# Performance work log

Hardware: AMD Instinct MI355X
Metric: run time of the kernel (lower is better)

## Reference

```python
import jax, jax.numpy as jnp
import numpy as np

NEG = -9e15  # mask value used by dense GAT implementations
BN_EPS = 1e-5


def gat_layer(x, W, a_src, a_dst, adj_mask):
    # Dense-adjacency GAT layer (pyGAT GraphAttentionLayer math).
    Wh = x @ W                                              # [N, H]
    e = jax.nn.leaky_relu(
        (Wh @ a_src)[:, None] + (Wh @ a_dst)[None, :], 0.2)  # [N, N]
    scores = jnp.where(adj_mask, e, NEG)
    att = jax.nn.softmax(scores, axis=1)                    # scatter-softmax over neighbors
    return att @ Wh                                         # [N, H]


def batchnorm(h, gamma, beta):
    # BatchNorm1d in training mode: biased batch stats over the node axis.
    mu = h.mean(axis=0)
    var = h.var(axis=0)
    return gamma * (h - mu) * jax.lax.rsqrt(var + BN_EPS) + beta


def setup_inputs() -> dict:
    key = jax.random.key(0)
    ks = jax.random.split(key, 8)
    N, F, H = 4096, 512, 256
    x = jax.random.normal(ks[0], (N, F), dtype=jnp.float32)
    adj = jax.random.randint(ks[1], (N, N), 0, 2, dtype=jnp.int32)
    W1 = jax.random.normal(ks[2], (F, H), dtype=jnp.float32) / np.sqrt(F)
    a1_src = jax.random.normal(ks[3], (H,), dtype=jnp.float32) / np.sqrt(H)
    a1_dst = jax.random.normal(ks[4], (H,), dtype=jnp.float32) / np.sqrt(H)
    W2 = jax.random.normal(ks[5], (H, H), dtype=jnp.float32) / np.sqrt(H)
    a2_src = jax.random.normal(ks[6], (H,), dtype=jnp.float32) / np.sqrt(H)
    a2_dst = jax.random.normal(ks[7], (H,), dtype=jnp.float32) / np.sqrt(H)
    return {
        "x": x, "adj": adj,
        "W1": W1, "a1_src": a1_src, "a1_dst": a1_dst,
        "gamma1": jnp.ones((H,), jnp.float32), "beta1": jnp.zeros((H,), jnp.float32),
        "W2": W2, "a2_src": a2_src, "a2_dst": a2_dst,
        "gamma2": jnp.ones((H,), jnp.float32), "beta2": jnp.zeros((H,), jnp.float32),
    }


def reference(x, adj, W1, a1_src, a1_dst, gamma1, beta1,
              W2, a2_src, a2_dst, gamma2, beta2):
    adj_mask = adj > 0
    h = jax.nn.relu(gat_layer(x, W1, a1_src, a1_dst, adj_mask))
    h = batchnorm(h, gamma1, beta1)
    # dropout is identity at inference time (deterministic reference)
    h = jax.nn.relu(gat_layer(h, W2, a2_src, a2_dst, adj_mask))
    h = batchnorm(h, gamma2, beta2)
    return h
```

## Files before the change

kernel.cpp:

```cpp
#include <hip/hip_runtime.h>

#define LOG2E 1.4426950408889634f

typedef unsigned long long u64;
typedef unsigned int uint;
typedef unsigned short ushort_t;
typedef __attribute__((ext_vector_type(8))) short short8;
typedef __attribute__((ext_vector_type(4))) float floatx4;
typedef __attribute__((ext_vector_type(4))) int intx4;
typedef __attribute__((ext_vector_type(4))) unsigned short ushort4v;

#define GN 4096
#define GH 256
#define KZ 8
#define KSTEPS 16

__device__ __forceinline__ ushort_t f2bf(float f){
  uint u = __float_as_uint(f);
  u += 0x7FFFu + ((u >> 16) & 1u);
  return (ushort_t)(u >> 16);
}
__device__ __forceinline__ float bf2f(ushort_t h){
  return __uint_as_float(((uint)h) << 16);
}
__device__ __forceinline__ float exp2_(float x){
#if __has_builtin(__builtin_amdgcn_exp2f)
  return __builtin_amdgcn_exp2f(x);
#else
  return exp2f(x);
#endif
}

__global__ __launch_bounds__(256) void prep(const int* __restrict__ adj,
                                            u64* __restrict__ mask,
                                            const float* __restrict__ W1,
                                            ushort_t* __restrict__ W1h,
                                            ushort_t* __restrict__ W1l,
                                            const float* __restrict__ W2,
                                            ushort_t* __restrict__ W2h,
                                            ushort_t* __restrict__ W2l){
  __shared__ union {
    unsigned char nib[2][1024];
    ushort_t tt[2][32][33];
  } sh;
  const int t = threadIdx.x;
  if (blockIdx.x < 2048){
    const int r0 = blockIdx.x * 2;
    const int* base = adj + (size_t)r0 * GN;
    #pragma unroll
    for (int i = 0; i < 8; ++i){
      int c = i * 256 + t;
      intx4 v = *(const intx4*)(base + c * 4);
      uint n = (uint)(v[0] > 0) | ((uint)(v[1] > 0) << 1) |
               ((uint)(v[2] > 0) << 2) | ((uint)(v[3] > 0) << 3);
      sh.nib[c >> 10][c & 1023] = (unsigned char)n;
    }
    __syncthreads();
    if (t < 128){
      int r = t >> 6, wi = t & 63;
      const u64* p = (const u64*)sh.nib[r];
      u64 x0 = p[wi * 2], x1 = p[wi * 2 + 1];
      auto comp = [](u64 x)->u64{
        x = (x | (x >> 4))  & 0x00FF00FF00FF00FFULL;
        x = (x | (x >> 8))  & 0x0000FFFF0000FFFFULL;
        x = (x | (x >> 16)) & 0x00000000FFFFFFFFULL;
        return x;
      };
      mask[(size_t)(r0 + r) * 64 + wi] = comp(x0) | (comp(x1) << 32);
    }
    return;
  }
  int b = blockIdx.x - 2048;
  const float* in; ushort_t* hi; ushort_t* lo; int R, idx;
  if (b < 128){ in = W1; hi = W1h; lo = W1l; R = 512; idx = b; }
  else        { in = W2; hi = W2h; lo = W2l; R = 256; idx = b - 128; }
  const int C = GH;
  const int bx = idx & 7, by = idx >> 3;
  const int i0 = by * 32, j0 = bx * 32;
  const int r = t >> 3, c4 = (t & 7) * 4;
  floatx4 v = *(const floatx4*)(in + (size_t)(i0 + r) * C + j0 + c4);
  #pragma unroll
  for (int e = 0; e < 4; ++e){
    ushort_t h = f2bf(v[e]);
    sh.tt[0][r][c4 + e] = h;
    sh.tt[1][r][c4 + e] = f2bf(v[e] - bf2f(h));
  }
  __syncthreads();
  ushort4v oh, ol;
  #pragma unroll
  for (int e = 0; e < 4; ++e){ oh[e] = sh.tt[0][c4 + e][r]; ol[e] = sh.tt[1][c4 + e][r]; }
  *(ushort4v*)(hi + (size_t)(j0 + r) * R + i0 + c4) = oh;
  *(ushort4v*)(lo + (size_t)(j0 + r) * R + i0 + c4) = ol;
}

template<bool BN>
__global__ __launch_bounds__(256) void gemm_split(const float* __restrict__ A,
                                                  const ushort_t* __restrict__ BThi,
                                                  const ushort_t* __restrict__ BTlo,
                                                  const float* __restrict__ bnsc,
                                                  const float* __restrict__ bnbi,
                                                  float* __restrict__ Cf, int K){
  __shared__ short8 AhiV[32 * 8];
  __shared__ short8 AloV[32 * 8];
  __shared__ short8 BhiV[64 * 8];
  __shared__ short8 BloV[64 * 8];
  char* Ahi = (char*)AhiV; char* Alo = (char*)AloV;
  char* Bhi = (char*)BhiV; char* Blo = (char*)BloV;
  const int tid = threadIdx.x;
  const int i0 = blockIdx.y * 32, n0 = blockIdx.x * 64;
  const int lane = tid & 63, wave = tid >> 6;
  const int wr = wave & 1, wc = wave >> 1;
  const int l15 = lane & 15, lhi = lane >> 4;
  const int rs = tid >> 3, ch = tid & 7;
  floatx4 acc[2] = {};
  for (int kb = 0; kb < K; kb += 64){
    {
      int r = rs;
      floatx4 f0 = *(const floatx4*)(A + (size_t)(i0 + r) * K + kb + ch * 8);
      floatx4 f1 = *(const floatx4*)(A + (size_t)(i0 + r) * K + kb + ch * 8 + 4);
      if constexpr (BN){
        floatx4 sc0 = *(const floatx4*)(bnsc + kb + ch * 8);
        floatx4 sc1 = *(const floatx4*)(bnsc + kb + ch * 8 + 4);
        floatx4 bi0 = *(const floatx4*)(bnbi + kb + ch * 8);
        floatx4 bi1 = *(const floatx4*)(bnbi + kb + ch * 8 + 4);
        #pragma unroll
        for (int e = 0; e < 4; ++e){
          f0[e] = f0[e] * sc0[e] + bi0[e];
          f1[e] = f1[e] * sc1[e] + bi1[e];
        }
      }
      short8 ah, al;
      #pragma unroll
      for (int e = 0; e < 4; ++e){
        ushort_t h0 = f2bf(f0[e]); ah[e] = (short)h0; al[e] = (short)f2bf(f0[e] - bf2f(h0));
        ushort_t h1 = f2bf(f1[e]); ah[e+4] = (short)h1; al[e+4] = (short)f2bf(f1[e] - bf2f(h1));
      }
      const int sw = (ch * 16) ^ ((r & 7) << 4);
      *(short8*)(Ahi + r * 128 + sw) = ah;
      *(short8*)(Alo + r * 128 + sw) = al;
      #pragma unroll
      for (int q = 0; q < 2; ++q){
        int rb = rs + q * 32;
        const int swb = (ch * 16) ^ ((rb & 7) << 4);
        short8 bh = *(const short8*)(BThi + (size_t)(n0 + rb) * K + kb + ch * 8);
        short8 bl = *(const short8*)(BTlo + (size_t)(n0 + rb) * K + kb + ch * 8);
        *(short8*)(Bhi + rb * 128 + swb) = bh;
        *(short8*)(Blo + rb * 128 + swb) = bl;
      }
    }
    __syncthreads();
    #pragma unroll
    for (int kt = 0; kt < 2; ++kt){
      int klb = (kt * 32 + lhi * 8) * 2;
      int rowA = wr * 16 + l15;
      int swA = klb ^ ((rowA & 7) << 4);
      short8 ah = *(const short8*)(Ahi + rowA * 128 + swA);
      short8 al = *(const short8*)(Alo + rowA * 128 + swA);
      #pragma unroll
      for (int n = 0; n < 2; ++n){
        int rowB = wc * 32 + n * 16 + l15;
        int swB = klb ^ ((rowB & 7) << 4);
        short8 bh = *(const short8*)(Bhi + rowB * 128 + swB);
        short8 bl = *(const short8*)(Blo + rowB * 128 + swB);
        acc[n] = __builtin_amdgcn_mfma_f32_16x16x32_bf16(ah, bh, acc[n], 0, 0, 0);
        acc[n] = __builtin_amdgcn_mfma_f32_16x16x32_bf16(ah, bl, acc[n], 0, 0, 0);
        acc[n] = __builtin_amdgcn_mfma_f32_16x16x32_bf16(al, bh, acc[n], 0, 0, 0);
      }
    }
    __syncthreads();
  }
  #pragma unroll
  for (int rr = 0; rr < 4; ++rr){
    int row = i0 + wr * 16 + lhi * 4 + rr;
    #pragma unroll
    for (int n = 0; n < 2; ++n){
      int col = n0 + wc * 32 + n * 16 + l15;
      Cf[(size_t)row * GH + col] = acc[n][rr];
    }
  }
}

__global__ __launch_bounds__(256) void skthi(const float* __restrict__ Whf,
                                             const float* __restrict__ asrc,
                                             const float* __restrict__ adst,
                                             float* __restrict__ ss,
                                             float* __restrict__ sd,
                                             ushort_t* __restrict__ VTh){
  __shared__ ushort_t tile[256][36];
  const int tid = threadIdx.x;
  const int i0 = blockIdx.x * 32;
  const int r = tid >> 3, cg = tid & 7;
  float s = 0.f, d = 0.f;
  #pragma unroll
  for (int j = 0; j < 8; ++j){
    int col = j * 32 + cg * 4;
    floatx4 v = *(const floatx4*)(Whf + (size_t)(i0 + r) * GH + col);
    floatx4 s4 = *(const floatx4*)(asrc + col);
    floatx4 d4 = *(const floatx4*)(adst + col);
    #pragma unroll
    for (int e = 0; e < 4; ++e){
      s += v[e] * s4[e]; d += v[e] * d4[e];
      tile[col + e][r] = f2bf(v[e]);
    }
  }
  #pragma unroll
  for (int off = 1; off < 8; off <<= 1){
    s += __shfl_xor(s, off);
    d += __shfl_xor(d, off);
  }
  if (cg == 0){ ss[i0 + r] = s * LOG2E; sd[i0 + r] = d * LOG2E; }
  __syncthreads();
  const int rr4 = (tid & 7) * 4, cb = tid >> 3;
  #pragma unroll
  for (int ct = 0; ct < 8; ++ct){
    int col = ct * 32 + cb;
    ushort4v o = *(const ushort4v*)(&tile[col][rr4]);
    *(ushort4v*)(VTh + (size_t)col * GN + i0 + rr4) = o;
  }
}

__global__ __launch_bounds__(128, 2) void gat_pv(const u64* __restrict__ mask,
                                                 const float* __restrict__ ss,
                                                 const float* __restrict__ sd,
                                                 const ushort_t* __restrict__ VTh,
                                                 float* __restrict__ partial,
                                                 float* __restrict__ szb){
  __shared__ char Blds[2][20480];
  const int tid = threadIdx.x;
  const int lane = tid & 63, w = tid >> 6;
  const int l15 = lane & 15, lhi = lane >> 4;
  const int i0 = blockIdx.x * 32;
  const int kz = blockIdx.y;
  const int ch = tid & 3, c0 = tid >> 2;
  const int ncol0 = w * 128;

  const int row0 = i0 + l15;
  const int row1 = i0 + 16 + l15;
  const float ss0 = ss[row0], ss1 = ss[row1];

  u64 mw0[8], mw1[8];
  {
    const u64* mr0 = mask + (size_t)row0 * 64 + kz * 8;
    const u64* mr1 = mask + (size_t)row1 * 64 + kz * 8;
    #pragma unroll
    for (int q = 0; q < 8; ++q){ mw0[q] = mr0[q]; mw1[q] = mr1[q]; }
  }

  floatx4 acc[2][8] = {};
  float srow0 = 0.f, srow1 = 0.f;
  short8 g[8];

  auto GLOAD = [&](int kb){
    const int kbase = (kz * KSTEPS + kb) * 32;
    #pragma unroll
    for (int i = 0; i < 8; ++i){
      int c = c0 + 32 * i;
      g[i] = *(const short8*)(VTh + (size_t)c * GN + kbase + ch * 8);
    }
  };
  auto SWRITE = [&](int buf){
    #pragma unroll
    for (int i = 0; i < 8; ++i){
      int c = c0 + 32 * i;
      *(short8*)(Blds[buf] + c * 80 + ch * 16) = g[i];
    }
  };

  GLOAD(0); SWRITE(0); __syncthreads();

  for (int kb = 0; kb < KSTEPS; ++kb){
    if (kb + 1 < KSTEPS) GLOAD(kb + 1);

    const int kbase = (kz * KSTEPS + kb) * 32;
    floatx4 s0 = *(const floatx4*)(sd + kbase + lhi * 8);
    floatx4 s1 = *(const floatx4*)(sd + kbase + lhi * 8 + 4);
    const int sh = ((kb & 1) << 5) + lhi * 8;
    uint b0 = (uint)(mw0[kb >> 1] >> sh) & 0xffu;
    uint b1 = (uint)(mw1[kb >> 1] >> sh) & 0xffu;
    short8 a0, a1;
    #pragma unroll
    for (int e = 0; e < 8; ++e){
      float sv = (e < 4) ? s0[e] : s1[e - 4];
      float t0 = ss0 + sv, t1 = ss1 + sv;
      float lr0 = fmaxf(t0, 0.2f * t0), lr1 = fmaxf(t1, 0.2f * t1);
      float p0 = exp2_(lr0), p1 = exp2_(lr1);
      p0 = ((b0 >> e) & 1u) ? p0 : 0.0f;
      p1 = ((b1 >> e) & 1u) ? p1 : 0.0f;
      srow0 += p0; srow1 += p1;
      a0[e] = (short)f2bf(p0);
      a1[e] = (short)f2bf(p1);
    }

    const char* B = Blds[kb & 1];
    #pragma unroll
    for (int n = 0; n < 8; ++n){
      short8 b = *(const short8*)(B + (ncol0 + n * 16 + l15) * 80 + lhi * 16);
      acc[0][n] = __builtin_amdgcn_mfma_f32_16x16x32_bf16(a0, b, acc[0][n], 0, 0, 0);
      acc[1][n] = __builtin_amdgcn_mfma_f32_16x16x32_bf16(a1, b, acc[1][n], 0, 0, 0);
    }

    if (kb + 1 < KSTEPS){
      SWRITE((kb + 1) & 1);
      __syncthreads();
    }
  }

  srow0 += __shfl_xor(srow0, 16); srow0 += __shfl_xor(srow0, 32);
  srow1 += __shfl_xor(srow1, 16); srow1 += __shfl_xor(srow1, 32);
  if (w == 0 && lhi == 0){
    szb[(size_t)kz * GN + row0] = srow0;
    szb[(size_t)kz * GN + row1] = srow1;
  }

  float* pout = partial + (size_t)kz * GN * GH;
  #pragma unroll
  for (int m = 0; m < 2; ++m){
    const int rbase = i0 + m * 16 + lhi * 4;
    #pragma unroll
    for (int n = 0; n < 8; ++n){
      int col = ncol0 + n * 16 + l15;
      #pragma unroll
      for (int rr = 0; rr < 4; ++rr)
        pout[(size_t)(rbase + rr) * GH + col] = acc[m][n][rr];
    }
  }
}

__global__ __launch_bounds__(256) void combine_colpart(const float* __restrict__ partial,
                                                       const float* __restrict__ szb,
                                                       float* __restrict__ outb,
                                                       float* __restrict__ part,
                                                       float* __restrict__ partm2){
  __shared__ float fl[4];
  __shared__ float sm[4][GH];
  const int tid = threadIdx.x;
  const int b = blockIdx.x;
  const int r0 = b * 4;
  if (tid < 4){
    int row = r0 + tid;
    float lsum = 0.f;
    #pragma unroll
    for (int z = 0; z < 8; ++z) lsum += szb[(size_t)z * GN + row];
    fl[tid] = lsum > 0.f ? 1.0f / lsum : 0.f;
  }
  __syncthreads();
  const int r = tid >> 6;
  const int c4 = (tid & 63) * 4;
  const size_t idx = (size_t)(r0 + r) * GH + c4;
  floatx4 x = {};
  #pragma unroll
  for (int z = 0; z < 8; ++z){
    floatx4 p = *(const floatx4*)(partial + (size_t)z * GN * GH + idx);
    #pragma unroll
    for (int e = 0; e < 4; ++e) x[e] += p[e];
  }
  const float linv = fl[r];
  #pragma unroll
  for (int e = 0; e < 4; ++e) x[e] = fmaxf(x[e] * linv, 0.0f);
  *(floatx4*)(outb + idx) = x;
  *(floatx4*)(&sm[r][c4]) = x;
  __syncthreads();
  if (tid < 64){
    const int cb = tid * 4;
    floatx4 v0 = *(const floatx4*)(&sm[0][cb]);
    floatx4 v1 = *(const floatx4*)(&sm[1][cb]);
    floatx4 v2 = *(const floatx4*)(&sm[2][cb]);
    floatx4 v3 = *(const floatx4*)(&sm[3][cb]);
    floatx4 s, m2;
    #pragma unroll
    for (int e = 0; e < 4; ++e){
      float sum = v0[e] + v1[e] + v2[e] + v3[e];
      float mu = sum * 0.25f;
      float d0 = v0[e]-mu, d1 = v1[e]-mu, d2 = v2[e]-mu, d3 = v3[e]-mu;
      s[e] = sum;
      m2[e] = d0*d0 + d1*d1 + d2*d2 + d3*d3;
    }
    *(floatx4*)(part + (size_t)b * GH + cb) = s;
    *(floatx4*)(partm2 + (size_t)b * GH + cb) = m2;
  }
}

__global__ __launch_bounds__(256) void colfin(const float* __restrict__ part,
                                              const float* __restrict__ partm2,
                                              const float* __restrict__ gamma,
                                              const float* __restrict__ beta,
                                              float* __restrict__ scale,
                                              float* __restrict__ bias){
  __shared__ double red[8][33];
  const int cl = threadIdx.x & 31, g = threadIdx.x >> 5;
  const int c = blockIdx.x * 32 + cl;
  double S = 0.0;
  for (int b = g * 128; b < g * 128 + 128; ++b) S += (double)part[(size_t)b * GH + c];
  red[g][cl] = S;
  __syncthreads();
  double mean = 0.0;
  #pragma unroll
  for (int q = 0; q < 8; ++q) mean += red[q][cl];
  mean *= (1.0 / 4096.0);
  double M2 = 0.0;
  for (int b = g * 128; b < g * 128 + 128; ++b){
    double mb = (double)part[(size_t)b * GH + c] * 0.25;
    double dd = mb - mean;
    M2 += (double)partm2[(size_t)b * GH + c] + 4.0 * dd * dd;
  }
  __syncthreads();
  red[g][cl] = M2;
  __syncthreads();
  if (g == 0){
    double M2t = 0.0;
    #pragma unroll
    for (int q = 0; q < 8; ++q) M2t += red[q][cl];
    double var = M2t * (1.0 / 4096.0);
    float sc = gamma[c] * (float)(1.0 / sqrt(var + 1e-5));
    scale[c] = sc;
    bias[c] = beta[c] - (float)mean * sc;
  }
}

__global__ __launch_bounds__(256) void bnapply(const float* __restrict__ outb,
                                               const float* __restrict__ scale,
                                               const float* __restrict__ bias,
                                               float* __restrict__ dst){
  const int base = (blockIdx.x * 256 + threadIdx.x) * 4;
  const int c = base & (GH - 1);
  floatx4 v = *(const floatx4*)(outb + base);
  floatx4 s = *(const floatx4*)(scale + c);
  floatx4 b = *(const floatx4*)(bias + c);
  #pragma unroll
  for (int e = 0; e < 4; ++e) v[e] = v[e] * s[e] + b[e];
  *(floatx4*)(dst + base) = v;
}

extern "C" void kernel_launch(void* const* d_in, const int* in_sizes, int n_in,
                              void* d_out, int out_size, void* d_ws, size_t ws_size,
                              hipStream_t stream) {
  const float* x      = (const float*)d_in[0];
  const int*   adj    = (const int*)d_in[1];
  const float* W1     = (const float*)d_in[2];
  const float* a1s    = (const float*)d_in[3];
  const float* a1d    = (const float*)d_in[4];
  const float* g1     = (const float*)d_in[5];
  const float* b1     = (const float*)d_in[6];
  const float* W2     = (const float*)d_in[7];
  const float* a2s    = (const float*)d_in[8];
  const float* a2d    = (const float*)d_in[9];
  const float* g2     = (const float*)d_in[10];
  const float* b2     = (const float*)d_in[11];

  char* w = (char*)d_ws;
  auto alloc = [&](size_t bytes){ void* p = (void*)w; w += (bytes + 255) & ~(size_t)255; return p; };
  u64*      mask   = (u64*)alloc((size_t)GN * 64 * 8);
  ushort_t* W1Th   = (ushort_t*)alloc((size_t)GH * 512 * 2);
  ushort_t* W1Tl   = (ushort_t*)alloc((size_t)GH * 512 * 2);
  ushort_t* W2Th   = (ushort_t*)alloc((size_t)GH * GH * 2);
  ushort_t* W2Tl   = (ushort_t*)alloc((size_t)GH * GH * 2);
  float*    Whf    = (float*)alloc((size_t)GN * GH * 4);
  ushort_t* VThb   = (ushort_t*)alloc((size_t)GH * GN * 2);
  float*    outb   = (float*)alloc((size_t)GN * GH * 4);
  float*    partial= (float*)alloc((size_t)KZ * GN * GH * 4);
  float*    ssb    = (float*)alloc(GN * 4);
  float*    sdb    = (float*)alloc(GN * 4);
  float*    szb    = (float*)alloc((size_t)KZ * GN * 4);
  float*    part   = (float*)alloc((size_t)1024 * GH * 4);
  float*    partm2 = (float*)alloc((size_t)1024 * GH * 4);
  float*    scale  = (float*)alloc(GH * 4);
  float*    bias   = (float*)alloc(GH * 4);

  prep<<<2048 + 192, 256, 0, stream>>>(adj, mask, W1, W1Th, W1Tl, W2, W2Th, W2Tl);

  gemm_split<false><<<dim3(4, 128), 256, 0, stream>>>(x, W1Th, W1Tl, nullptr, nullptr, Whf, 512);
  skthi<<<128, 256, 0, stream>>>(Whf, a1s, a1d, ssb, sdb, VThb);
  gat_pv<<<dim3(GN/32, KZ), 128, 0, stream>>>(mask, ssb, sdb, VThb, partial, szb);
  combine_colpart<<<1024, 256, 0, stream>>>(partial, szb, outb, part, partm2);
  colfin<<<8, 256, 0, stream>>>(part, partm2, g1, b1, scale, bias);

  gemm_split<true><<<dim3(4, 128), 256, 0, stream>>>(outb, W2Th, W2Tl, scale, bias, Whf, 256);
  skthi<<<128, 256, 0, stream>>>(Whf, a2s, a2d, ssb, sdb, VThb);
  gat_pv<<<dim3(GN/32, KZ), 128, 0, stream>>>(mask, ssb, sdb, VThb, partial, szb);
  combine_colpart<<<1024, 256, 0, stream>>>(partial, szb, outb, part, partm2);
  colfin<<<8, 256, 0, stream>>>(part, partm2, g2, b2, scale, bias);
  bnapply<<<1024, 256, 0, stream>>>(outb, scale, bias, (float*)d_out);
}
```

Before: 137.8 us.

## Share attention-weight computation across waves via LDS and pack 4 rows per prep block

In gat_pv, each wave used to compute exp/leaky-relu weights for all 32 rows itself, so both waves duplicated the work. Now each lane computes one row×8-column slice, writes it to an LDS P tile, and both waves read their MFMA A-operands from it. The B tile drops from double to single buffering, which adds two barriers per k-step and reduces overlap between global loads and MFMA. The prep mask kernel now handles 4 adjacency rows per block with all threads packing, halving the block count.

```diff
diff --git a/kernel.cpp b/kernel.cpp
--- a/kernel.cpp
+++ b/kernel.cpp
@@ -40,15 +40,15 @@
                                             ushort_t* __restrict__ W2h,
                                             ushort_t* __restrict__ W2l){
   __shared__ union {
-    unsigned char nib[2][1024];
+    unsigned char nib[4][1024];
     ushort_t tt[2][32][33];
   } sh;
   const int t = threadIdx.x;
-  if (blockIdx.x < 2048){
-    const int r0 = blockIdx.x * 2;
+  if (blockIdx.x < 1024){
+    const int r0 = blockIdx.x * 4;
     const int* base = adj + (size_t)r0 * GN;
     #pragma unroll
-    for (int i = 0; i < 8; ++i){
+    for (int i = 0; i < 16; ++i){
       int c = i * 256 + t;
       intx4 v = *(const intx4*)(base + c * 4);
       uint n = (uint)(v[0] > 0) | ((uint)(v[1] > 0) << 1) |
@@ -56,7 +56,7 @@
       sh.nib[c >> 10][c & 1023] = (unsigned char)n;
     }
     __syncthreads();
-    if (t < 128){
+    {
       int r = t >> 6, wi = t & 63;
       const u64* p = (const u64*)sh.nib[r];
       u64 x0 = p[wi * 2], x1 = p[wi * 2 + 1];
@@ -70,7 +70,7 @@
     }
     return;
   }
-  int b = blockIdx.x - 2048;
+  int b = blockIdx.x - 1024;
   const float* in; ushort_t* hi; ushort_t* lo; int R, idx;
   if (b < 128){ in = W1; hi = W1h; lo = W1l; R = 512; idx = b; }
   else        { in = W2; hi = W2h; lo = W2l; R = 256; idx = b - 128; }
@@ -219,13 +219,15 @@
   }
 }
 
-__global__ __launch_bounds__(128, 2) void gat_pv(const u64* __restrict__ mask,
-                                                 const float* __restrict__ ss,
-                                                 const float* __restrict__ sd,
-                                                 const ushort_t* __restrict__ VTh,
-                                                 float* __restrict__ partial,
-                                                 float* __restrict__ szb){
-  __shared__ char Blds[2][20480];
+__global__ __launch_bounds__(128) void gat_pv(const u64* __restrict__ mask,
+                                              const float* __restrict__ ss,
+                                              const float* __restrict__ sd,
+                                              const ushort_t* __restrict__ VTh,
+                                              float* __restrict__ partial,
+                                              float* __restrict__ szb){
+  __shared__ char Blds[20480];
+  __shared__ char Plds[32 * 80];
+  __shared__ float wsum[2][32];
   const int tid = threadIdx.x;
   const int lane = tid & 63, w = tid >> 6;
   const int l15 = lane & 15, lhi = lane >> 4;
@@ -234,20 +236,20 @@
   const int ch = tid & 3, c0 = tid >> 2;
   const int ncol0 = w * 128;
 
-  const int row0 = i0 + l15;
-  const int row1 = i0 + 16 + l15;
-  const float ss0 = ss[row0], ss1 = ss[row1];
-
-  u64 mw0[8], mw1[8];
+  const int prow = l15 + ((lhi & 1) << 4);
+  const int row = i0 + prow;
+  const float ssr = ss[row];
+  const int kkb = w * 16 + ((lhi >> 1) << 3);
+
+  u64 mw[8];
   {
-    const u64* mr0 = mask + (size_t)row0 * 64 + kz * 8;
-    const u64* mr1 = mask + (size_t)row1 * 64 + kz * 8;
-    #pragma unroll
-    for (int q = 0; q < 8; ++q){ mw0[q] = mr0[q]; mw1[q] = mr1[q]; }
+    const u64* mr = mask + (size_t)row * 64 + kz * 8;
+    #pragma unroll
+    for (int q = 0; q < 8; ++q) mw[q] = mr[q];
   }
 
   floatx4 acc[2][8] = {};
-  float srow0 = 0.f, srow1 = 0.f;
+  float srow = 0.f;
   short8 g[8];
 
   auto GLOAD = [&](int kb){
@@ -258,59 +260,57 @@
       g[i] = *(const short8*)(VTh + (size_t)c * GN + kbase + ch * 8);
     }
   };
-  auto SWRITE = [&](int buf){
+  auto SWRITE = [&](){
     #pragma unroll
     for (int i = 0; i < 8; ++i){
       int c = c0 + 32 * i;
-      *(short8*)(Blds[buf] + c * 80 + ch * 16) = g[i];
+      *(short8*)(Blds + c * 80 + ch * 16) = g[i];
     }
   };
 
-  GLOAD(0); SWRITE(0); __syncthreads();
+  GLOAD(0); SWRITE(); __syncthreads();
 
   for (int kb = 0; kb < KSTEPS; ++kb){
+    {
+      const int kbase = (kz * KSTEPS + kb) * 32;
+      floatx4 s0 = *(const floatx4*)(sd + kbase + kkb);
+      floatx4 s1 = *(const floatx4*)(sd + kbase + kkb + 4);
+      const int sh = ((kb & 1) << 5) + kkb;
+      uint bits = (uint)(mw[kb >> 1] >> sh) & 0xffu;
+      short8 pv;
+      #pragma unroll
+      for (int e = 0; e < 8; ++e){
+        float sv = (e < 4) ? s0[e] : s1[e - 4];
+        float t = ssr + sv;
+        float lr = fmaxf(t, 0.2f * t);
+        float p = exp2_(lr);
+        p = ((bits >> e) & 1u) ? p : 0.0f;
+        srow += p;
+        pv[e] = (short)f2bf(p);
+      }
+      *(short8*)(Plds + prow * 80 + kkb * 2) = pv;
+    }
+    __syncthreads();
+
     if (kb + 1 < KSTEPS) GLOAD(kb + 1);
 
-    const int kbase = (kz * KSTEPS + kb) * 32;
-    floatx4 s0 = *(const floatx4*)(sd + kbase + lhi * 8);
-    floatx4 s1 = *(const floatx4*)(sd + kbase + lhi * 8 + 4);
-    const int sh = ((kb & 1) << 5) + lhi * 8;
-    uint b0 = (uint)(mw0[kb >> 1] >> sh) & 0xffu;
-    uint b1 = (uint)(mw1[kb >> 1] >> sh) & 0xffu;
-    short8 a0, a1;
-    #pragma unroll
-    for (int e = 0; e < 8; ++e){
-      float sv = (e < 4) ? s0[e] : s1[e - 4];
-      float t0 = ss0 + sv, t1 = ss1 + sv;
-      float lr0 = fmaxf(t0, 0.2f * t0), lr1 = fmaxf(t1, 0.2f * t1);
-      float p0 = exp2_(lr0), p1 = exp2_(lr1);
-      p0 = ((b0 >> e) & 1u) ? p0 : 0.0f;
-      p1 = ((b1 >> e) & 1u) ? p1 : 0.0f;
-      srow0 += p0; srow1 += p1;
-      a0[e] = (short)f2bf(p0);
-      a1[e] = (short)f2bf(p1);
-    }
-
-    const char* B = Blds[kb & 1];
+    short8 a0 = *(const short8*)(Plds + l15 * 80 + lhi * 16);
+    short8 a1 = *(const short8*)(Plds + (l15 + 16) * 80 + lhi * 16);
     #pragma unroll
     for (int n = 0; n < 8; ++n){
-      short8 b = *(const short8*)(B + (ncol0 + n * 16 + l15) * 80 + lhi * 16);
+      short8 b = *(const short8*)(Blds + (ncol0 + n * 16 + l15) * 80 + lhi * 16);
       acc[0][n] = __builtin_amdgcn_mfma_f32_16x16x32_bf16(a0, b, acc[0][n], 0, 0, 0);
       acc[1][n] = __builtin_amdgcn_mfma_f32_16x16x32_bf16(a1, b, acc[1][n], 0, 0, 0);
     }
-
-    if (kb + 1 < KSTEPS){
-      SWRITE((kb + 1) & 1);
-      __syncthreads();
-    }
-  }
-
-  srow0 += __shfl_xor(srow0, 16); srow0 += __shfl_xor(srow0, 32);
-  srow1 += __shfl_xor(srow1, 16); srow1 += __shfl_xor(srow1, 32);
-  if (w == 0 && lhi == 0){
-    szb[(size_t)kz * GN + row0] = srow0;
-    szb[(size_t)kz * GN + row1] = srow1;
-  }
+    __syncthreads();
+    if (kb + 1 < KSTEPS) SWRITE();
+  }
+
+  srow += __shfl_xor(srow, 32);
+  if (lane < 32) wsum[w][prow] = srow;
+  __syncthreads();
+  if (w == 0 && lane < 32)
+    szb[(size_t)kz * GN + i0 + lane] = wsum[0][lane] + wsum[1][lane];
 
   float* pout = partial + (size_t)kz * GN * GH;
   #pragma unroll
@@ -466,7 +466,7 @@
   float*    scale  = (float*)alloc(GH * 4);
   float*    bias   = (float*)alloc(GH * 4);
 
-  prep<<<2048 + 192, 256, 0, stream>>>(adj, mask, W1, W1Th, W1Tl, W2, W2Th, W2Tl);
+  prep<<<1024 + 192, 256, 0, stream>>>(adj, mask, W1, W1Th, W1Tl, W2, W2Th, W2Tl);
 
   gemm_split<false><<<dim3(4, 128), 256, 0, stream>>>(x, W1Th, W1Tl, nullptr, nullptr, Whf, 512);
   skthi<<<128, 256, 0, stream>>>(Whf, a1s, a1d, ssb, sdb, VThb);
```

Result: no change. 137.8 us (+0.0%).
